# Kernel tuning notes

Hardware: AMD Instinct MI355X
Metric: run time of the kernel (lower is better)

Reference implementation:

```python
import jax, jax.numpy as jnp
import numpy as np

C_DIM = 768
NH = 12
MLP_HIDDEN = 3072


def _ln(x, g, b, eps=1e-5):
    mu = x.mean(-1, keepdims=True)
    var = ((x - mu) ** 2).mean(-1, keepdims=True)
    return (x - mu) / jnp.sqrt(var + eps) * g + b


def _mha(x, Wqkv, nh, scale):
    # x: [N, L, C]; Wqkv: [C, 3C] packed as (3, nh, hd) on output dim
    N, L, C = x.shape
    hd = C // nh
    qkv = (x @ Wqkv).reshape(N, L, 3, nh, hd)
    q, k, v = qkv[:, :, 0], qkv[:, :, 1], qkv[:, :, 2]  # [N, L, nh, hd]
    a = jnp.einsum('nqhd,nkhd->nhqk', q, k) * scale
    a = jax.nn.softmax(a, axis=-1)
    o = jnp.einsum('nhqk,nkhd->nqhd', a, v).reshape(N, L, C)
    return o


def setup_inputs() -> dict:
    key = jax.random.key(0)
    ks = jax.random.split(key, 16)
    B, T, K, C = 4, 16, 196, C_DIM
    s = 0.02
    inp = {
        'x': jax.random.normal(ks[0], (B, 1 + K * T, C), jnp.float32),
        'B': B, 'T': T, 'K': K,
        'ln1_g': jnp.ones((C,)), 'ln1_b': jnp.zeros((C,)),
        'lnt_g': jnp.ones((C,)), 'lnt_b': jnp.zeros((C,)),
        'ln2_g': jnp.ones((C,)), 'ln2_b': jnp.zeros((C,)),
        'lncls_g': jnp.ones((C,)), 'lncls_b': jnp.zeros((C,)),
        'Wqkv_s': jax.random.normal(ks[1], (C, 3 * C)) * s,
        'Wproj_s': jax.random.normal(ks[2], (C, C)) * s,
        'bproj_s': jnp.zeros((C,)),
        'Wqkv4': jax.random.normal(ks[3], (C, 3 * C)) * s,
        'Wqkv8': jax.random.normal(ks[4], (C, 3 * C)) * s,
        'Wqkv16': jax.random.normal(ks[5], (C, 3 * C)) * s,
        'Wp4': jax.random.normal(ks[6], (C, C)) * s, 'bp4': jnp.zeros((C,)),
        'Wp8': jax.random.normal(ks[7], (C, C)) * s, 'bp8': jnp.zeros((C,)),
        'Wp16': jax.random.normal(ks[8], (C, C)) * s, 'bp16': jnp.zeros((C,)),
        'Wtfc': jax.random.normal(ks[9], (C, C)) * s, 'btfc': jnp.zeros((C,)),
        'Wfc1': jax.random.normal(ks[10], (C, MLP_HIDDEN)) * s, 'bfc1': jnp.zeros((MLP_HIDDEN,)),
        'Wfc2': jax.random.normal(ks[11], (MLP_HIDDEN, C)) * s, 'bfc2': jnp.zeros((C,)),
    }
    return inp


def reference(x, B, T, K, ln1_g, ln1_b, lnt_g, lnt_b, ln2_g, ln2_b,
              lncls_g, lncls_b, Wqkv_s, Wproj_s, bproj_s,
              Wqkv4, Wqkv8, Wqkv16, Wp4, bp4, Wp8, bp8, Wp16, bp16,
              Wtfc, btfc, Wfc1, bfc1, Wfc2, bfc2):
    C = x.shape[-1]
    nh = NH
    scale = (C // nh) ** -0.5
    t1, t2 = T // 4, T // 2

    # ---- multi-scale temporal attention (eval mode: all dropout identity) ----
    xt = x[:, 1:, :].reshape(B, K, T, C).reshape(B * K, T, C)
    xt_n = _ln(xt, lnt_g, lnt_b)
    x4 = _mha(xt_n[:, T - t1:], Wqkv4, nh, scale) @ Wp4 + bp4    # [BK, t1, C]
    x8 = _mha(xt_n[:, t2:], Wqkv8, nh, scale) @ Wp8 + bp8        # [BK, t2, C]
    x16 = _mha(xt_n, Wqkv16, nh, scale) @ Wp16 + bp16            # [BK, T, C]
    # windowed fusion of overlapping scales
    x8 = jnp.concatenate([x8[:, :t1], 0.5 * x8[:, t1:] + 0.5 * x4], axis=1)
    x16 = jnp.concatenate([x16[:, :t2], 0.5 * x16[:, t2:] + 0.5 * x8], axis=1)
    res_temp = x16.reshape(B, K * T, C)
    xt_full = res_temp @ Wtfc + btfc + x[:, 1:, :]               # [B, K*T, C]

    # ---- spatial attention with replicated CLS token ----
    init_cls = x[:, 0:1, :]                                      # [B, 1, C]
    cls_rep = jnp.broadcast_to(init_cls, (B, T, C)).reshape(B * T, 1, C)
    xs = xt_full.reshape(B, K, T, C).transpose(0, 2, 1, 3).reshape(B * T, K, C)
    xs = jnp.concatenate([cls_rep, xs], axis=1)                  # [B*T, K+1, C]
    res_spatial = _mha(_ln(xs, ln1_g, ln1_b), Wqkv_s, nh, scale) @ Wproj_s + bproj_s

    # ---- CLS aggregation over time ----
    cls_sp = _ln(res_spatial[:, 0, :].reshape(B, T, C), lncls_g, lncls_b)
    target = cls_sp[:, -1:, :]                                   # [B, 1, C]
    attn2 = jax.nn.softmax(jnp.einsum('bqc,btc->bqt', target, cls_sp), axis=-1)
    cls_sp = attn2 @ cls_sp                                      # [B, 1, C]

    x_s = res_spatial[:, 1:, :].reshape(B, T, K, C).transpose(0, 2, 1, 3).reshape(B, K * T, C)
    x_cat = jnp.concatenate([init_cls, xt_full], axis=1) + jnp.concatenate([cls_sp, x_s], axis=1)

    # ---- MLP residual ----
    h = _ln(x_cat, ln2_g, ln2_b)
    h = jax.nn.gelu(h @ Wfc1 + bfc1, approximate=False) @ Wfc2 + bfc2
    return x_cat + h
```

## Files before the change

kernel.cpp:

```cpp
#include <hip/hip_runtime.h>
#include <hip/hip_bf16.h>
#include <stdint.h>

#define BF16 __hip_bfloat16

typedef __attribute__((ext_vector_type(8))) short short8;
typedef __attribute__((ext_vector_type(2))) short short2v;
typedef __attribute__((ext_vector_type(4))) float floatx4;

typedef const __attribute__((address_space(1))) void* gas_cvp;
typedef __attribute__((address_space(3))) void* las_vp;

__device__ __forceinline__ float bf2f(BF16 v) { return __bfloat162float(v); }
__device__ __forceinline__ BF16 f2bf(float v) { return __float2bfloat16(v); }

__global__ __launch_bounds__(256) void wtrans(const float* __restrict__ W,
                                              BF16* __restrict__ Wt, int K, int N) {
    __shared__ float t[32][33];
    int k0 = blockIdx.x * 32, n0 = blockIdx.y * 32;
    int tx = threadIdx.x & 31, ty = threadIdx.x >> 5;
#pragma unroll
    for (int i = 0; i < 32; i += 8) t[ty + i][tx] = W[(size_t)(k0 + ty + i) * N + n0 + tx];
    __syncthreads();
#pragma unroll
    for (int i = 0; i < 32; i += 8)
        Wt[(size_t)(n0 + ty + i) * K + k0 + tx] = f2bf(t[tx][ty + i]);
}

struct WTJob { const float* src; BF16* dst; int K; int N; int boff; };
struct WTParams { WTJob j[12]; };

__global__ __launch_bounds__(256) void wtrans_all(WTParams P) {
    __shared__ float t[32][33];
    const int bid = blockIdx.x;
    int ji = 0;
#pragma unroll
    for (int i = 1; i < 12; ++i)
        if (bid >= P.j[i].boff) ji = i;
    const float* __restrict__ W = P.j[ji].src;
    BF16* __restrict__ Wt = P.j[ji].dst;
    const int K = P.j[ji].K, N = P.j[ji].N;
    const int lb = bid - P.j[ji].boff;
    const int kb = K >> 5;
    const int k0 = (lb % kb) * 32, n0 = (lb / kb) * 32;
    const int tx = threadIdx.x & 31, ty = threadIdx.x >> 5;
#pragma unroll
    for (int i = 0; i < 32; i += 8) t[ty + i][tx] = W[(size_t)(k0 + ty + i) * N + n0 + tx];
    __syncthreads();
#pragma unroll
    for (int i = 0; i < 32; i += 8)
        Wt[(size_t)(n0 + ty + i) * K + k0 + tx] = f2bf(t[tx][ty + i]);
}

template <int MODE>
__global__ __launch_bounds__(256) void ln_kernel(const float* __restrict__ src0,
                                                 const float* __restrict__ src1,
                                                 const BF16* __restrict__ srcb,
                                                 const float* __restrict__ g,
                                                 const float* __restrict__ bta,
                                                 BF16* __restrict__ dst_bf,
                                                 float* __restrict__ dst_f) {
    const int r = blockIdx.x, tid = threadIdx.x;
    float x0, x1, x2;
    {
        const float* src;
        if (MODE == 0) {
            int b = r / 3136, rr = r - b * 3136;
            src = src0 + ((size_t)b * 3137 + 1 + rr) * 768;
        } else if (MODE == 1) {
            int bt = r / 197, j = r - bt * 197;
            int b = bt >> 4, t = bt & 15;
            if (j == 0) src = src0 + (size_t)b * 3137 * 768;
            else        src = src1 + ((size_t)(b * 3137 + 1) + (size_t)(j - 1) * 16 + t) * 768;
        } else {
            src = src0 + (size_t)r * 768;
        }
        x0 = src[tid]; x1 = src[tid + 256]; x2 = src[tid + 512];
    }
    float s = x0 + x1 + x2;
    float ss = x0 * x0 + x1 * x1 + x2 * x2;
    __shared__ float red[8];
#pragma unroll
    for (int o = 32; o > 0; o >>= 1) { s += __shfl_down(s, o); ss += __shfl_down(ss, o); }
    if ((tid & 63) == 0) { red[tid >> 6] = s; red[4 + (tid >> 6)] = ss; }
    __syncthreads();
    s = red[0] + red[1] + red[2] + red[3];
    ss = red[4] + red[5] + red[6] + red[7];
    const float mu = s * (1.0f / 768.0f);
    const float var = ss * (1.0f / 768.0f) - mu * mu;
    const float rstd = rsqrtf(var + 1e-5f);
#pragma unroll
    for (int i = 0; i < 3; ++i) {
        int c = tid + i * 256;
        float xv = (i == 0) ? x0 : (i == 1) ? x1 : x2;
        float y = (xv - mu) * rstd * g[c] + bta[c];
        dst_bf[(size_t)r * 768 + c] = f2bf(y);
    }
}

template <int AMAP, int OMODE>
__global__ __launch_bounds__(256) void gemm_bf16(const BF16* __restrict__ A,
                                                 const BF16* __restrict__ Bt,
                                                 const float* __restrict__ bias,
                                                 const void* res,
                                                 void* Cout,
                                                 int M, int N, int K) {
    __shared__ BF16 Al[128 * 64];
    __shared__ BF16 Bl[128 * 64];
    const int tid = threadIdx.x;
    const int lane = tid & 63;
    const int w = tid >> 6;

    const int gx = gridDim.x;
    const int nwg = gx * (int)gridDim.y;
    const int orig = (int)blockIdx.y * gx + (int)blockIdx.x;
    const int xcd = orig & 7;
    const int idx = orig >> 3;
    const int q8 = nwg >> 3, r8 = nwg & 7;
    const int wgid = (xcd < r8 ? xcd * (q8 + 1) : r8 * (q8 + 1) + (xcd - r8) * q8) + idx;
    const int bn0 = (wgid % gx) * 128;
    const int bm0 = (wgid / gx) * 128;

    const BF16* gsrc[8];
    BF16* ldst[8];
    const int rin = lane >> 3;
    const int kblk = (lane & 7) ^ rin;
#pragma unroll
    for (int j = 0; j < 8; ++j) {
        int c = w * 8 + j;
        if (c < 16) {
            int gr = bm0 + c * 8 + rin;
            if (gr > M - 1) gr = M - 1;
            if (AMAP == 1) gr = (gr >> 3) * 16 + 8 + (gr & 7);
            if (AMAP == 2) gr = (gr >> 2) * 16 + 12 + (gr & 3);
            gsrc[j] = A + (size_t)gr * K + kblk * 8;
            ldst[j] = Al + c * 512;
        } else {
            int gn = bn0 + (c - 16) * 8 + rin;
            gsrc[j] = Bt + (size_t)gn * K + kblk * 8;
            ldst[j] = Bl + (c - 16) * 512;
        }
    }

    const int wm = (w & 1) * 64;
    const int wn = (w >> 1) * 64;
    const int fr = lane & 15;
    const int fq = lane >> 4;
    const int sw = fr & 7;
    const int o0 = (fq ^ sw) * 8;
    const int o1 = ((fq + 4) ^ sw) * 8;
    const BF16* pa[4];
    const BF16* pb[4];
#pragma unroll
    for (int t = 0; t < 4; ++t) {
        pa[t] = Al + (wm + t * 16 + fr) * 64;
        pb[t] = Bl + (wn + t * 16 + fr) * 64;
    }

    floatx4 acc[4][4];
#pragma unroll
    for (int i = 0; i < 4; ++i)
#pragma unroll
        for (int j = 0; j < 4; ++j) acc[i][j] = (floatx4){0.f, 0.f, 0.f, 0.f};

    for (int k0 = 0; k0 < K; k0 += 64) {
#pragma unroll
        for (int j = 0; j < 8; ++j) {
            __builtin_amdgcn_global_load_lds((gas_cvp)gsrc[j], (las_vp)ldst[j], 16, 0, 0);
            gsrc[j] += 64;
        }
        __syncthreads();
        {
            short8 af[4], bfr[4];
#pragma unroll
            for (int t = 0; t < 4; ++t) {
                af[t] = *(const short8*)(pa[t] + o0);
                bfr[t] = *(const short8*)(pb[t] + o0);
            }
#pragma unroll
            for (int mt = 0; mt < 4; ++mt)
#pragma unroll
                for (int nt = 0; nt < 4; ++nt)
                    acc[mt][nt] = __builtin_amdgcn_mfma_f32_16x16x32_bf16(af[mt], bfr[nt], acc[mt][nt], 0, 0, 0);
#pragma unroll
            for (int t = 0; t < 4; ++t) {
                af[t] = *(const short8*)(pa[t] + o1);
                bfr[t] = *(const short8*)(pb[t] + o1);
            }
#pragma unroll
            for (int mt = 0; mt < 4; ++mt)
#pragma unroll
                for (int nt = 0; nt < 4; ++nt)
                    acc[mt][nt] = __builtin_amdgcn_mfma_f32_16x16x32_bf16(af[mt], bfr[nt], acc[mt][nt], 0, 0, 0);
        }
        __syncthreads();
    }

#pragma unroll
    for (int mt = 0; mt < 4; ++mt) {
#pragma unroll
        for (int nt = 0; nt < 4; ++nt) {
            const int gcol = bn0 + wn + nt * 16 + fr;
#pragma unroll
            for (int r = 0; r < 4; ++r) {
                const int grow = bm0 + wm + mt * 16 + fq * 4 + r;
                if (grow < M) {
                    float v = acc[mt][nt][r];
                    if (OMODE != 0 && OMODE != 8) v += bias[gcol];
                    if (OMODE == 0 || OMODE == 1) {
                        ((BF16*)Cout)[(size_t)grow * N + gcol] = f2bf(v);
                    } else if (OMODE == 2) {
                        int t8 = grow & 7;
                        int rr = (grow >> 3) * 16 + 8 + t8;
                        float w8 = (t8 < 4) ? 0.5f : 0.25f;
                        BF16* R = (BF16*)Cout;
                        size_t o = (size_t)rr * 768 + gcol;
                        R[o] = f2bf(0.5f * bf2f(R[o]) + w8 * v);
                    } else if (OMODE == 3) {
                        int t4 = grow & 3;
                        int rr = (grow >> 2) * 16 + 12 + t4;
                        BF16* R = (BF16*)Cout;
                        size_t o = (size_t)rr * 768 + gcol;
                        R[o] = f2bf(bf2f(R[o]) + 0.25f * v);
                    } else if (OMODE == 4) {
                        int b = grow / 3136;
                        size_t xrow = (size_t)b * 3137 + 1 + (grow - b * 3136);
                        ((float*)Cout)[xrow * 768 + gcol] =
                            v + ((const float*)res)[xrow * 768 + gcol];
                    } else if (OMODE == 6) {
                        float u = v * (0.7978845608f + 0.0356774081f * v * v);
                        v = v / (1.0f + __expf(-2.0f * u));
                        ((BF16*)Cout)[(size_t)grow * N + gcol] = f2bf(v);
                    } else {
                        v += ((const float*)res)[(size_t)grow * N + gcol];
                        ((float*)Cout)[(size_t)grow * N + gcol] = v;
                    }
                }
            }
        }
    }
}

template <int L, int NT>
__global__ __launch_bounds__(NT) void temporal_attn(const BF16* __restrict__ qkv,
                                                    BF16* __restrict__ outp) {
    __shared__ float q[L * 64];
    __shared__ float k[L * 65];
    __shared__ float v[L * 64];
    __shared__ float S[L * L];
    const int bh = blockIdx.x;
    const int b = bh / 12, h = bh % 12;
    const int tid = threadIdx.x;
    const size_t rb = (size_t)b * L;
    for (int idx = tid; idx < L * 64; idx += NT) {
        int i = idx >> 6, d = idx & 63;
        size_t base = (rb + i) * 2304 + h * 64 + d;
        q[i * 64 + d] = bf2f(qkv[base]);
        k[i * 65 + d] = bf2f(qkv[base + 768]);
        v[i * 64 + d] = bf2f(qkv[base + 1536]);
    }
    __syncthreads();
    for (int idx = tid; idx < L * L; idx += NT) {
        int i = idx / L, j = idx % L;
        float a = 0.f;
#pragma unroll
        for (int d = 0; d < 64; ++d) a += q[i * 64 + d] * k[j * 65 + d];
        S[idx] = a * 0.125f;
    }
    __syncthreads();
    if (tid < L) {
        float mx = -1e30f;
        for (int j = 0; j < L; ++j) mx = fmaxf(mx, S[tid * L + j]);
        float sm = 0.f;
        for (int j = 0; j < L; ++j) { float e = __expf(S[tid * L + j] - mx); S[tid * L + j] = e; sm += e; }
        float inv = 1.0f / sm;
        for (int j = 0; j < L; ++j) S[tid * L + j] *= inv;
    }
    __syncthreads();
    for (int idx = tid; idx < L * 64; idx += NT) {
        int i = idx >> 6, d = idx & 63;
        float acc = 0.f;
#pragma unroll
        for (int j = 0; j < L; ++j) acc += S[i * L + j] * v[j * 64 + d];
        outp[(rb + i) * 768 + h * 64 + d] = f2bf(acc);
    }
}

__global__ __launch_bounds__(256) void spatial_attn_mfma(const BF16* __restrict__ qkv,
                                                         BF16* __restrict__ outp) {
    const int bid = blockIdx.x;
    const int qt = bid & 3;
    const int h = (bid >> 2) % 12;
    const int bt = bid / 48;
    const int rowbase = bt * 197;
    __shared__ BF16 Ks[208 * 72];
    __shared__ BF16 Vt[64 * 232];
    __shared__ BF16 Pl[4][16 * 232];
    const int tid = threadIdx.x;
    const int lane = tid & 63;
    const int w = tid >> 6;
    const int ln = lane & 15;
    const int quad = lane >> 4;

    for (int it = tid; it < 208 * 8; it += 256) {
        int key = it >> 3, c = it & 7;
        int kc = key < 197 ? key : 196;
        short8 gk = *(const short8*)(qkv + (size_t)(rowbase + kc) * 2304 + 768 + h * 64 + c * 8);
        *(short8*)&Ks[key * 72 + c * 8] = gk;
    }
    for (int it = tid; it < 112 * 8; it += 256) {
        int p = it >> 3, c = it & 7;
        int kc0 = (2 * p < 197) ? 2 * p : 196;
        int kc1 = (2 * p + 1 < 197) ? 2 * p + 1 : 196;
        short8 a = *(const short8*)(qkv + (size_t)(rowbase + kc0) * 2304 + 1536 + h * 64 + c * 8);
        short8 b = *(const short8*)(qkv + (size_t)(rowbase + kc1) * 2304 + 1536 + h * 64 + c * 8);
#pragma unroll
        for (int e = 0; e < 8; ++e) {
            short2v pr;
            pr[0] = a[e];
            pr[1] = b[e];
            *(short2v*)&Vt[(c * 8 + e) * 232 + 2 * p] = pr;
        }
    }
    __syncthreads();

    const int m0 = qt * 64 + w * 16;
    int qrow = m0 + ln; if (qrow > 196) qrow = 196;
    const BF16* qptr = qkv + (size_t)(rowbase + qrow) * 2304 + h * 64 + quad * 8;
    short8 aq0 = *(const short8*)(qptr);
    short8 aq1 = *(const short8*)(qptr + 32);

    floatx4 sacc[13];
#pragma unroll
    for (int nt = 0; nt < 13; ++nt) sacc[nt] = (floatx4){0.f, 0.f, 0.f, 0.f};
#pragma unroll
    for (int nt = 0; nt < 13; ++nt) {
        const BF16* kb = &Ks[(nt * 16 + ln) * 72 + quad * 8];
        short8 b0 = *(const short8*)kb;
        short8 b1 = *(const short8*)(kb + 32);
        sacc[nt] = __builtin_amdgcn_mfma_f32_16x16x32_bf16(aq0, b0, sacc[nt], 0, 0, 0);
        sacc[nt] = __builtin_amdgcn_mfma_f32_16x16x32_bf16(aq1, b1, sacc[nt], 0, 0, 0);
    }

#pragma unroll
    for (int r = 0; r < 4; ++r) {
        float mx = -1e30f;
#pragma unroll
        for (int nt = 0; nt < 13; ++nt) {
            float s = sacc[nt][r] * 0.125f;
            sacc[nt][r] = s;
            if (nt * 16 + ln < 197) mx = fmaxf(mx, s);
        }
        mx = fmaxf(mx, __shfl_xor(mx, 1));
        mx = fmaxf(mx, __shfl_xor(mx, 2));
        mx = fmaxf(mx, __shfl_xor(mx, 4));
        mx = fmaxf(mx, __shfl_xor(mx, 8));
        float sum = 0.f;
#pragma unroll
        for (int nt = 0; nt < 13; ++nt) {
            float e = (nt * 16 + ln < 197) ? __expf(sacc[nt][r] - mx) : 0.f;
            sacc[nt][r] = e;
            sum += e;
        }
        sum += __shfl_xor(sum, 1);
        sum += __shfl_xor(sum, 2);
        sum += __shfl_xor(sum, 4);
        sum += __shfl_xor(sum, 8);
        float inv = 1.0f / sum;
#pragma unroll
        for (int nt = 0; nt < 13; ++nt) sacc[nt][r] *= inv;
    }

    BF16* pw = Pl[w];
#pragma unroll
    for (int nt = 0; nt < 13; ++nt)
#pragma unroll
        for (int r = 0; r < 4; ++r)
            pw[(quad * 4 + r) * 232 + nt * 16 + ln] = f2bf(sacc[nt][r]);
#pragma unroll
    for (int r = 0; r < 4; ++r)
        pw[(quad * 4 + r) * 232 + 208 + ln] = f2bf(0.f);

    floatx4 oacc[4];
#pragma unroll
    for (int nt = 0; nt < 4; ++nt) oacc[nt] = (floatx4){0.f, 0.f, 0.f, 0.f};
    for (int kb = 0; kb < 7; ++kb) {
        short8 ap = *(const short8*)&pw[ln * 232 + kb * 32 + quad * 8];
#pragma unroll
        for (int nt = 0; nt < 4; ++nt) {
            short8 bv = *(const short8*)&Vt[(nt * 16 + ln) * 232 + kb * 32 + quad * 8];
            oacc[nt] = __builtin_amdgcn_mfma_f32_16x16x32_bf16(ap, bv, oacc[nt], 0, 0, 0);
        }
    }

#pragma unroll
    for (int nt = 0; nt < 4; ++nt) {
        int dim = nt * 16 + ln;
#pragma unroll
        for (int r = 0; r < 4; ++r) {
            int q = m0 + quad * 4 + r;
            if (q < 197)
                outp[(size_t)(rowbase + q) * 768 + h * 64 + dim] = f2bf(oacc[nt][r]);
        }
    }
}

__global__ __launch_bounds__(256) void cls_ln_attn_kernel(const BF16* __restrict__ res_sp,
                                                          const float* __restrict__ g,
                                                          const float* __restrict__ bta,
                                                          float* __restrict__ clsout) {
    const int b = blockIdx.x;
    const int tid = threadIdx.x;
    __shared__ float sLN[16][768];
    __shared__ float red[8];
    __shared__ float dots[16];
    __shared__ float aw[16];

    for (int t = 0; t < 16; ++t) {
        const BF16* src = res_sp + (size_t)((b * 16 + t) * 197) * 768;
        float x0 = bf2f(src[tid]);
        float x1 = bf2f(src[tid + 256]);
        float x2 = bf2f(src[tid + 512]);
        float s = x0 + x1 + x2;
        float ss = x0 * x0 + x1 * x1 + x2 * x2;
#pragma unroll
        for (int o = 32; o > 0; o >>= 1) { s += __shfl_down(s, o); ss += __shfl_down(ss, o); }
        if ((tid & 63) == 0) { red[tid >> 6] = s; red[4 + (tid >> 6)] = ss; }
        __syncthreads();
        s = red[0] + red[1] + red[2] + red[3];
        ss = red[4] + red[5] + red[6] + red[7];
        const float mu = s * (1.0f / 768.0f);
        const float var = ss * (1.0f / 768.0f) - mu * mu;
        const float rstd = rsqrtf(var + 1e-5f);
        sLN[t][tid]       = (x0 - mu) * rstd * g[tid] + bta[tid];
        sLN[t][tid + 256] = (x1 - mu) * rstd * g[tid + 256] + bta[tid + 256];
        sLN[t][tid + 512] = (x2 - mu) * rstd * g[tid + 512] + bta[tid + 512];
        __syncthreads();
    }

    const int t = tid >> 4, l16 = tid & 15;
    float p = 0.f;
    for (int c = l16; c < 768; c += 16) p += sLN[15][c] * sLN[t][c];
#pragma unroll
    for (int o = 8; o > 0; o >>= 1) p += __shfl_down(p, o, 16);
    if (l16 == 0) dots[t] = p;
    __syncthreads();
    if (tid == 0) {
        float mx = -1e30f;
        for (int j = 0; j < 16; ++j) mx = fmaxf(mx, dots[j]);
        float s = 0.f;
        for (int j = 0; j < 16; ++j) { aw[j] = __expf(dots[j] - mx); s += aw[j]; }
        float inv = 1.0f / s;
        for (int j = 0; j < 16; ++j) aw[j] *= inv;
    }
    __syncthreads();
    for (int c = tid; c < 768; c += 256) {
        float acc = 0.f;
#pragma unroll
        for (int j = 0; j < 16; ++j) acc += aw[j] * sLN[j][c];
        clsout[(size_t)b * 768 + c] = acc;
    }
}

__global__ __launch_bounds__(256) void xcat_ln_kernel(const float* __restrict__ x,
                                                      const BF16* __restrict__ res_sp,
                                                      const float* __restrict__ clsout,
                                                      const float* __restrict__ g,
                                                      const float* __restrict__ bta,
                                                      float* outbuf,
                                                      BF16* __restrict__ hln) {
    const int gidx = blockIdx.x;
    const int b = gidx / 3137, j = gidx - b * 3137;
    const int tid = threadIdx.x;
    float v0, v1, v2;
    if (j == 0) {
        const float* xr = x + (size_t)b * 3137 * 768;
        const float* cr = clsout + (size_t)b * 768;
        v0 = xr[tid] + cr[tid];
        v1 = xr[tid + 256] + cr[tid + 256];
        v2 = xr[tid + 512] + cr[tid + 512];
    } else {
        const int p = j - 1, k = p >> 4, t = p & 15;
        const BF16* rs = res_sp + (size_t)((b * 16 + t) * 197 + 1 + k) * 768;
        float* orow = outbuf + (size_t)gidx * 768;
        v0 = orow[tid] + bf2f(rs[tid]);
        v1 = orow[tid + 256] + bf2f(rs[tid + 256]);
        v2 = orow[tid + 512] + bf2f(rs[tid + 512]);
    }
    float* orow = outbuf + (size_t)gidx * 768;
    orow[tid] = v0; orow[tid + 256] = v1; orow[tid + 512] = v2;

    float s = v0 + v1 + v2;
    float ss = v0 * v0 + v1 * v1 + v2 * v2;
    __shared__ float red[8];
#pragma unroll
    for (int o = 32; o > 0; o >>= 1) { s += __shfl_down(s, o); ss += __shfl_down(ss, o); }
    if ((tid & 63) == 0) { red[tid >> 6] = s; red[4 + (tid >> 6)] = ss; }
    __syncthreads();
    s = red[0] + red[1] + red[2] + red[3];
    ss = red[4] + red[5] + red[6] + red[7];
    const float mu = s * (1.0f / 768.0f);
    const float var = ss * (1.0f / 768.0f) - mu * mu;
    const float rstd = rsqrtf(var + 1e-5f);
#pragma unroll
    for (int i = 0; i < 3; ++i) {
        int c = tid + i * 256;
        float xv = (i == 0) ? v0 : (i == 1) ? v1 : v2;
        hln[(size_t)gidx * 768 + c] = f2bf((xv - mu) * rstd * g[c] + bta[c]);
    }
}

extern "C" void kernel_launch(void* const* d_in, const int* in_sizes, int n_in,
                              void* d_out, int out_size, void* d_ws, size_t ws_size,
                              hipStream_t stream) {
    const float* x       = (const float*)d_in[0];
    const float* ln1_g   = (const float*)d_in[4];
    const float* ln1_b   = (const float*)d_in[5];
    const float* lnt_g   = (const float*)d_in[6];
    const float* lnt_b   = (const float*)d_in[7];
    const float* ln2_g   = (const float*)d_in[8];
    const float* ln2_b   = (const float*)d_in[9];
    const float* lncls_g = (const float*)d_in[10];
    const float* lncls_b = (const float*)d_in[11];
    const float* Wqkv_s  = (const float*)d_in[12];
    const float* Wproj_s = (const float*)d_in[13];
    const float* bproj_s = (const float*)d_in[14];
    const float* Wqkv4   = (const float*)d_in[15];
    const float* Wqkv8   = (const float*)d_in[16];
    const float* Wqkv16  = (const float*)d_in[17];
    const float* Wp4     = (const float*)d_in[18];
    const float* bp4     = (const float*)d_in[19];
    const float* Wp8     = (const float*)d_in[20];
    const float* bp8     = (const float*)d_in[21];
    const float* Wp16    = (const float*)d_in[22];
    const float* bp16    = (const float*)d_in[23];
    const float* Wtfc    = (const float*)d_in[24];
    const float* btfc    = (const float*)d_in[25];
    const float* Wfc1    = (const float*)d_in[26];
    const float* bfc1    = (const float*)d_in[27];
    const float* Wfc2    = (const float*)d_in[28];
    const float* bfc2    = (const float*)d_in[29];
    float* out = (float*)d_out;

    const size_t oW0 = 0;
    const size_t oW1 = 4718592;
    const size_t oR1 = 9437184;
    const size_t oR2 = 28803072;
    const size_t oR3 = 48070656;
    const size_t oR4 = 77119488;
    const size_t oCO = 96681984;
    const size_t NEED = 96694272;
    const size_t NEED_BIG = NEED + 29491200;
    if (ws_size < NEED) return;
    char* ws = (char*)d_ws;

    BF16* w0       = (BF16*)(ws + oW0);
    BF16* w1       = (BF16*)(ws + oW1);
    BF16* xtn      = (BF16*)(ws + oR1);
    BF16* atts     = (BF16*)(ws + oR1);
    BF16* hln      = (BF16*)(ws + oR1);
    BF16* res_temp = (BF16*)(ws + oR2);
    BF16* h1       = (BF16*)(ws + oR2);
    BF16* qkv      = (BF16*)(ws + oR3);
    BF16* att      = (BF16*)(ws + oR4);
    BF16* xsn      = (BF16*)(ws + oR4);
    BF16* res_sp   = (BF16*)(ws + oR4);
    float* clsout  = (float*)(ws + oCO);

    const bool big = (ws_size >= NEED_BIG);
    BF16 *tqkv16, *tqkv8, *tqkv4, *tqkvs, *tp16, *tp8, *tp4, *ttfc, *tproj, *tfc1, *tfc2;
    if (big) {
        char* wx = ws + NEED;
        tqkv16 = (BF16*)wx; wx += 3538944;
        tqkv8  = (BF16*)wx; wx += 3538944;
        tqkv4  = (BF16*)wx; wx += 3538944;
        tqkvs  = (BF16*)wx; wx += 3538944;
        tp16   = (BF16*)wx; wx += 1179648;
        tp8    = (BF16*)wx; wx += 1179648;
        tp4    = (BF16*)wx; wx += 1179648;
        ttfc   = (BF16*)wx; wx += 1179648;
        tproj  = (BF16*)wx; wx += 1179648;
        tfc1   = (BF16*)wx; wx += 4718592;
        tfc2   = (BF16*)wx; wx += 4718592;
        WTParams P;
        P.j[0]  = { Wqkv16,                     tqkv16,                     768, 2304,     0 };
        P.j[1]  = { Wqkv8,                      tqkv8,                      768, 2304,  1728 };
        P.j[2]  = { Wqkv4,                      tqkv4,                      768, 2304,  3456 };
        P.j[3]  = { Wqkv_s,                     tqkvs,                      768, 2304,  5184 };
        P.j[4]  = { Wp16,                       tp16,                       768,  768,  6912 };
        P.j[5]  = { Wp8,                        tp8,                        768,  768,  7488 };
        P.j[6]  = { Wp4,                        tp4,                        768,  768,  8064 };
        P.j[7]  = { Wtfc,                       ttfc,                       768,  768,  8640 };
        P.j[8]  = { Wproj_s,                    tproj,                      768,  768,  9216 };
        P.j[9]  = { Wfc1,                       tfc1,                       768, 3072,  9792 };
        P.j[10] = { Wfc2,                       tfc2,                      1536,  768, 12096 };
        P.j[11] = { Wfc2 + (size_t)1536 * 768,  tfc2 + (size_t)768 * 1536, 1536,  768, 13248 };
        wtrans_all<<<14400, 256, 0, stream>>>(P);
    } else {
        tqkv16 = w0; tqkv8 = w0; tqkv4 = w0; tqkvs = w1;
        tp16 = w1; tp8 = w1; tp4 = w1; ttfc = w0; tproj = w0;
        tfc1 = w0; tfc2 = w1;
    }

    ln_kernel<0><<<12544, 256, 0, stream>>>(x, nullptr, nullptr, lnt_g, lnt_b, xtn, nullptr);

    if (!big) wtrans<<<dim3(24, 72), 256, 0, stream>>>(Wqkv16, tqkv16, 768, 2304);
    for (int c = 0; c < 2; ++c) {
        gemm_bf16<0, 0><<<dim3(18, 49), 256, 0, stream>>>(xtn + (size_t)c * 6272 * 768, tqkv16, nullptr, nullptr, qkv, 6272, 2304, 768);
        temporal_attn<16, 256><<<4704, 256, 0, stream>>>(qkv, att + (size_t)c * 6272 * 768);
    }
    if (!big) wtrans<<<dim3(24, 24), 256, 0, stream>>>(Wp16, tp16, 768, 768);
    gemm_bf16<0, 1><<<dim3(6, 98), 256, 0, stream>>>(att, tp16, bp16, nullptr, res_temp, 12544, 768, 768);

    if (!big) wtrans<<<dim3(24, 72), 256, 0, stream>>>(Wqkv8, tqkv8, 768, 2304);
    gemm_bf16<1, 0><<<dim3(18, 49), 256, 0, stream>>>(xtn, tqkv8, nullptr, nullptr, qkv, 6272, 2304, 768);
    temporal_attn<8, 64><<<9408, 64, 0, stream>>>(qkv, att);
    if (!big) wtrans<<<dim3(24, 24), 256, 0, stream>>>(Wp8, tp8, 768, 768);
    gemm_bf16<0, 2><<<dim3(6, 49), 256, 0, stream>>>(att, tp8, bp8, nullptr, res_temp, 6272, 768, 768);

    if (!big) wtrans<<<dim3(24, 72), 256, 0, stream>>>(Wqkv4, tqkv4, 768, 2304);
    gemm_bf16<2, 0><<<dim3(18, 25), 256, 0, stream>>>(xtn, tqkv4, nullptr, nullptr, qkv, 3136, 2304, 768);
    temporal_attn<4, 64><<<9408, 64, 0, stream>>>(qkv, att);
    if (!big) wtrans<<<dim3(24, 24), 256, 0, stream>>>(Wp4, tp4, 768, 768);
    gemm_bf16<0, 3><<<dim3(6, 25), 256, 0, stream>>>(att, tp4, bp4, nullptr, res_temp, 3136, 768, 768);

    if (!big) wtrans<<<dim3(24, 24), 256, 0, stream>>>(Wtfc, ttfc, 768, 768);
    gemm_bf16<0, 4><<<dim3(6, 98), 256, 0, stream>>>(res_temp, ttfc, btfc, x, out, 12544, 768, 768);

    ln_kernel<1><<<12608, 256, 0, stream>>>(x, out, nullptr, ln1_g, ln1_b, xsn, nullptr);
    if (!big) wtrans<<<dim3(24, 72), 256, 0, stream>>>(Wqkv_s, tqkvs, 768, 2304);
    for (int c = 0; c < 2; ++c) {
        gemm_bf16<0, 0><<<dim3(18, 50), 256, 0, stream>>>(xsn + (size_t)c * 6304 * 768, tqkvs, nullptr, nullptr, qkv, 6304, 2304, 768);
        spatial_attn_mfma<<<1536, 256, 0, stream>>>(qkv, atts + (size_t)c * 6304 * 768);
    }
    if (!big) wtrans<<<dim3(24, 24), 256, 0, stream>>>(Wproj_s, tproj, 768, 768);
    gemm_bf16<0, 1><<<dim3(6, 99), 256, 0, stream>>>(atts, tproj, bproj_s, nullptr, res_sp, 12608, 768, 768);

    cls_ln_attn_kernel<<<4, 256, 0, stream>>>(res_sp, lncls_g, lncls_b, clsout);

    xcat_ln_kernel<<<12548, 256, 0, stream>>>(x, res_sp, clsout, ln2_g, ln2_b, out, hln);

    if (!big) {
        wtrans<<<dim3(24, 96), 256, 0, stream>>>(Wfc1, tfc1, 768, 3072);
        wtrans<<<dim3(48, 24), 256, 0, stream>>>(Wfc2, tfc2, 1536, 768);
        wtrans<<<dim3(48, 24), 256, 0, stream>>>(Wfc2 + (size_t)1536 * 768, tfc2 + (size_t)768 * 1536, 1536, 768);
    }

    gemm_bf16<0, 6><<<dim3(12, 99), 256, 0, stream>>>(hln, tfc1, bfc1, nullptr, h1, 12548, 1536, 768);
    gemm_bf16<0, 7><<<dim3(6, 99), 256, 0, stream>>>(h1, tfc2, bfc2, out, out, 12548, 768, 1536);
    gemm_bf16<0, 6><<<dim3(12, 99), 256, 0, stream>>>(hln, tfc1 + (size_t)1536 * 768, bfc1 + 1536, nullptr, h1, 12548, 1536, 768);
    gemm_bf16<0, 8><<<dim3(6, 99), 256, 0, stream>>>(h1, tfc2 + (size_t)768 * 1536, nullptr, out, out, 12548, 768, 1536);
}
```

Baseline: 1.032 ms.

## Merge independent projection and next-scale QKV GEMMs into dual launches; alias spatial LDS

Pairs each temporal output-projection GEMM with the following, independent QKV GEMM for the next scale in a single grid that dispatches on block index. This cuts kernel launches and fills the tail of the smaller GEMM with blocks from the larger one. Separately, the spatial attention kernel reuses the K shared buffer for the per-wave P tiles after a barrier, which lowers LDS use and may allow higher occupancy. The cost is an extra __syncthreads in spatial attention and a shared code path that both templates must fit.

```diff
diff --git a/kernel.cpp b/kernel.cpp
--- a/kernel.cpp
+++ b/kernel.cpp
@@ -99,21 +99,17 @@
 }
 
 template <int AMAP, int OMODE>
-__global__ __launch_bounds__(256) void gemm_bf16(const BF16* __restrict__ A,
-                                                 const BF16* __restrict__ Bt,
-                                                 const float* __restrict__ bias,
-                                                 const void* res,
-                                                 void* Cout,
-                                                 int M, int N, int K) {
-    __shared__ BF16 Al[128 * 64];
-    __shared__ BF16 Bl[128 * 64];
+__device__ __forceinline__ void gemm_body(BF16* Al, BF16* Bl,
+                                          int orig, int nwg, int gx,
+                                          const BF16* __restrict__ A,
+                                          const BF16* __restrict__ Bt,
+                                          const float* __restrict__ bias,
+                                          const void* res, void* Cout,
+                                          int M, int N, int K) {
     const int tid = threadIdx.x;
     const int lane = tid & 63;
     const int w = tid >> 6;
 
-    const int gx = gridDim.x;
-    const int nwg = gx * (int)gridDim.y;
-    const int orig = (int)blockIdx.y * gx + (int)blockIdx.x;
     const int xcd = orig & 7;
     const int idx = orig >> 3;
     const int q8 = nwg >> 3, r8 = nwg & 7;
@@ -241,6 +237,39 @@
     }
 }
 
+template <int AMAP, int OMODE>
+__global__ __launch_bounds__(256) void gemm_bf16(const BF16* __restrict__ A,
+                                                 const BF16* __restrict__ Bt,
+                                                 const float* __restrict__ bias,
+                                                 const void* res,
+                                                 void* Cout,
+                                                 int M, int N, int K) {
+    __shared__ BF16 Al[128 * 64];
+    __shared__ BF16 Bl[128 * 64];
+    const int gx = gridDim.x;
+    const int nwg = gx * (int)gridDim.y;
+    const int orig = (int)blockIdx.y * gx + (int)blockIdx.x;
+    gemm_body<AMAP, OMODE>(Al, Bl, orig, nwg, gx, A, Bt, bias, res, Cout, M, N, K);
+}
+
+template <int AMAP0, int OMODE0, int AMAP1, int OMODE1>
+__global__ __launch_bounds__(256) void gemm_dual(
+        int nblk0, int gx0,
+        const BF16* A0, const BF16* B0, const float* b0, const void* r0, void* C0,
+        int M0, int N0, int K0,
+        int gx1,
+        const BF16* A1, const BF16* B1, const float* b1, const void* r1, void* C1,
+        int M1, int N1, int K1) {
+    __shared__ BF16 Al[128 * 64];
+    __shared__ BF16 Bl[128 * 64];
+    const int bid = blockIdx.x;
+    if (bid < nblk0)
+        gemm_body<AMAP0, OMODE0>(Al, Bl, bid, nblk0, gx0, A0, B0, b0, r0, C0, M0, N0, K0);
+    else
+        gemm_body<AMAP1, OMODE1>(Al, Bl, bid - nblk0, (int)gridDim.x - nblk0, gx1,
+                                 A1, B1, b1, r1, C1, M1, N1, K1);
+}
+
 template <int L, int NT>
 __global__ __launch_bounds__(NT) void temporal_attn(const BF16* __restrict__ qkv,
                                                     BF16* __restrict__ outp) {
@@ -293,9 +322,8 @@
     const int h = (bid >> 2) % 12;
     const int bt = bid / 48;
     const int rowbase = bt * 197;
-    __shared__ BF16 Ks[208 * 72];
+    __shared__ BF16 KsPl[208 * 72];
     __shared__ BF16 Vt[64 * 232];
-    __shared__ BF16 Pl[4][16 * 232];
     const int tid = threadIdx.x;
     const int lane = tid & 63;
     const int w = tid >> 6;
@@ -306,7 +334,7 @@
         int key = it >> 3, c = it & 7;
         int kc = key < 197 ? key : 196;
         short8 gk = *(const short8*)(qkv + (size_t)(rowbase + kc) * 2304 + 768 + h * 64 + c * 8);
-        *(short8*)&Ks[key * 72 + c * 8] = gk;
+        *(short8*)&KsPl[key * 72 + c * 8] = gk;
     }
     for (int it = tid; it < 112 * 8; it += 256) {
         int p = it >> 3, c = it & 7;
@@ -335,12 +363,13 @@
     for (int nt = 0; nt < 13; ++nt) sacc[nt] = (floatx4){0.f, 0.f, 0.f, 0.f};
 #pragma unroll
     for (int nt = 0; nt < 13; ++nt) {
-        const BF16* kb = &Ks[(nt * 16 + ln) * 72 + quad * 8];
+        const BF16* kb = &KsPl[(nt * 16 + ln) * 72 + quad * 8];
         short8 b0 = *(const short8*)kb;
         short8 b1 = *(const short8*)(kb + 32);
         sacc[nt] = __builtin_amdgcn_mfma_f32_16x16x32_bf16(aq0, b0, sacc[nt], 0, 0, 0);
         sacc[nt] = __builtin_amdgcn_mfma_f32_16x16x32_bf16(aq1, b1, sacc[nt], 0, 0, 0);
     }
+    __syncthreads();
 
 #pragma unroll
     for (int r = 0; r < 4; ++r) {
@@ -371,7 +400,7 @@
         for (int nt = 0; nt < 13; ++nt) sacc[nt][r] *= inv;
     }
 
-    BF16* pw = Pl[w];
+    BF16* pw = KsPl + w * (16 * 232);
 #pragma unroll
     for (int nt = 0; nt < 13; ++nt)
 #pragma unroll
@@ -609,18 +638,25 @@
         gemm_bf16<0, 0><<<dim3(18, 49), 256, 0, stream>>>(xtn + (size_t)c * 6272 * 768, tqkv16, nullptr, nullptr, qkv, 6272, 2304, 768);
         temporal_attn<16, 256><<<4704, 256, 0, stream>>>(qkv, att + (size_t)c * 6272 * 768);
     }
-    if (!big) wtrans<<<dim3(24, 24), 256, 0, stream>>>(Wp16, tp16, 768, 768);
-    gemm_bf16<0, 1><<<dim3(6, 98), 256, 0, stream>>>(att, tp16, bp16, nullptr, res_temp, 12544, 768, 768);
-
-    if (!big) wtrans<<<dim3(24, 72), 256, 0, stream>>>(Wqkv8, tqkv8, 768, 2304);
-    gemm_bf16<1, 0><<<dim3(18, 49), 256, 0, stream>>>(xtn, tqkv8, nullptr, nullptr, qkv, 6272, 2304, 768);
+
+    if (!big) {
+        wtrans<<<dim3(24, 24), 256, 0, stream>>>(Wp16, tp16, 768, 768);
+        wtrans<<<dim3(24, 72), 256, 0, stream>>>(Wqkv8, tqkv8, 768, 2304);
+    }
+    gemm_dual<0, 1, 1, 0><<<588 + 882, 256, 0, stream>>>(
+        588, 6, att, tp16, bp16, nullptr, res_temp, 12544, 768, 768,
+        18, xtn, tqkv8, nullptr, nullptr, qkv, 6272, 2304, 768);
     temporal_attn<8, 64><<<9408, 64, 0, stream>>>(qkv, att);
-    if (!big) wtrans<<<dim3(24, 24), 256, 0, stream>>>(Wp8, tp8, 768, 768);
-    gemm_bf16<0, 2><<<dim3(6, 49), 256, 0, stream>>>(att, tp8, bp8, nullptr, res_temp, 6272, 768, 768);
-
-    if (!big) wtrans<<<dim3(24, 72), 256, 0, stream>>>(Wqkv4, tqkv4, 768, 2304);
-    gemm_bf16<2, 0><<<dim3(18, 25), 256, 0, stream>>>(xtn, tqkv4, nullptr, nullptr, qkv, 3136, 2304, 768);
+
+    if (!big) {
+        wtrans<<<dim3(24, 24), 256, 0, stream>>>(Wp8, tp8, 768, 768);
+        wtrans<<<dim3(24, 72), 256, 0, stream>>>(Wqkv4, tqkv4, 768, 2304);
+    }
+    gemm_dual<0, 2, 2, 0><<<294 + 450, 256, 0, stream>>>(
+        294, 6, att, tp8, bp8, nullptr, res_temp, 6272, 768, 768,
+        18, xtn, tqkv4, nullptr, nullptr, qkv, 3136, 2304, 768);
     temporal_attn<4, 64><<<9408, 64, 0, stream>>>(qkv, att);
+
     if (!big) wtrans<<<dim3(24, 24), 256, 0, stream>>>(Wp4, tp4, 768, 768);
     gemm_bf16<0, 3><<<dim3(6, 25), 256, 0, stream>>>(att, tp4, bp4, nullptr, res_temp, 3136, 768, 768);
 
```

Measured after the change: 942.5 us. 8.6% less time.
